# Kernel tuning notes

Hardware: AMD Instinct MI355X
Metric: run time of the kernel (lower is better)

The kernel has to match this reference:

```python
import jax, jax.numpy as jnp
import numpy as np


def setup_inputs() -> dict:
    key = jax.random.key(0)
    k1, k2 = jax.random.split(key)
    B, N, C = 128, 200000, 100
    values = jax.random.normal(k1, (B, N), dtype=jnp.float32)
    labels = jax.random.randint(k2, (N,), 0, C, dtype=jnp.int64)
    return {"values": values, "labels": labels, "num_classes": C}


def reference(values, labels, num_classes):
    # Stratified (label-grouped) max pooling:
    # values: [B, N], labels: [N] in [0, num_classes)
    # output: [B, num_classes], out[b, c] = max over columns j with labels[j] == c
    # segment_max reduces over the leading axis, so operate on values.T [N, B].
    pooled = jax.ops.segment_max(
        values.T, labels, num_segments=num_classes, indices_are_sorted=False
    )  # [C, B]
    return pooled.T  # [B, C]
```

## Files before the change

### kernel.cpp

```cpp
#include <hip/hip_runtime.h>
#include <hip/hip_bf16.h>


#define TPB   256
#define ROWS  8
#define CHUNK 4096
#define CPAD  257

#define ENC_NEG_INF 0x007FFFFFu

__device__ __forceinline__ unsigned enc(float f) {
    unsigned u = __float_as_uint(f);
    return (u & 0x80000000u) ? ~u : (u | 0x80000000u);
}
__device__ __forceinline__ float dec(unsigned u) {
    unsigned b = (u & 0x80000000u) ? (u & 0x7FFFFFFFu) : ~u;
    return __uint_as_float(b);
}

__global__ __launch_bounds__(TPB) void strat_init(unsigned* __restrict__ out_enc, int n) {
    int i = blockIdx.x * TPB + threadIdx.x;
    if (i < n) out_enc[i] = ENC_NEG_INF;
}

__global__ __launch_bounds__(TPB) void strat_main(
    const float* __restrict__ values, const int* __restrict__ labels,
    unsigned* __restrict__ out_enc, int B, int N, int C) {
    __shared__ unsigned acc[ROWS * CPAD];

    const int tid    = threadIdx.x;
    const int chunk0 = blockIdx.x * CHUNK;
    const int row0   = blockIdx.y * ROWS;

    for (int i = tid; i < ROWS * CPAD; i += TPB) acc[i] = ENC_NEG_INF;
    __syncthreads();

    const int rmax = min(ROWS, B - row0);
    const bool full_chunk = (chunk0 + CHUNK <= N);

    if (full_chunk) {
        int4 L[4];
#pragma unroll
        for (int k = 0; k < 4; ++k)
            L[k] = ((const int4*)(labels + chunk0 + k * 1024))[tid];

        if (rmax == ROWS) {
#pragma unroll
            for (int r = 0; r < ROWS; ++r) {
                const float4* src =
                    (const float4*)(values + (size_t)(row0 + r) * N + chunk0) + tid;
                float4 v[4];
#pragma unroll
                for (int k = 0; k < 4; ++k) v[k] = src[k * 256];
                unsigned* accr = acc + r * CPAD;
#pragma unroll
                for (int k = 0; k < 4; ++k) {
                    atomicMax(&accr[L[k].x], enc(v[k].x));
                    atomicMax(&accr[L[k].y], enc(v[k].y));
                    atomicMax(&accr[L[k].z], enc(v[k].z));
                    atomicMax(&accr[L[k].w], enc(v[k].w));
                }
            }
        } else {
            for (int r = 0; r < rmax; ++r) {
                const float4* src =
                    (const float4*)(values + (size_t)(row0 + r) * N + chunk0) + tid;
                float4 v[4];
#pragma unroll
                for (int k = 0; k < 4; ++k) v[k] = src[k * 256];
                unsigned* accr = acc + r * CPAD;
#pragma unroll
                for (int k = 0; k < 4; ++k) {
                    atomicMax(&accr[L[k].x], enc(v[k].x));
                    atomicMax(&accr[L[k].y], enc(v[k].y));
                    atomicMax(&accr[L[k].z], enc(v[k].z));
                    atomicMax(&accr[L[k].w], enc(v[k].w));
                }
            }
        }
    } else {
        for (int r = 0; r < rmax; ++r) {
            unsigned* accr = acc + r * CPAD;
            const size_t rowoff = (size_t)(row0 + r) * N;
            for (int k = 0; k < 4; ++k) {
                int j = chunk0 + k * 1024 + tid * 4;
#pragma unroll
                for (int e = 0; e < 4; ++e) {
                    if (j + e < N) {
                        int c = labels[j + e];
                        atomicMax(&accr[c], enc(values[rowoff + j + e]));
                    }
                }
            }
        }
    }

    __syncthreads();

    for (int i = tid; i < rmax * C; i += TPB) {
        int r = i / C, c = i - r * C;
        atomicMax(&out_enc[(size_t)(row0 + r) * C + c], acc[r * CPAD + c]);
    }
}

__global__ __launch_bounds__(TPB) void strat_decode(unsigned* __restrict__ buf, int n) {
    int i = blockIdx.x * TPB + threadIdx.x;
    if (i < n) {
        float f = dec(buf[i]);
        ((float*)buf)[i] = f;
    }
}

extern "C" void kernel_launch(void* const* d_in, const int* in_sizes, int n_in,
                              void* d_out, int out_size, void* d_ws, size_t ws_size,
                              hipStream_t stream) {
    const float* values = (const float*)d_in[0];
    const int*   labels = (const int*)d_in[1];
    const int N = in_sizes[1];
    const int B = in_sizes[0] / N;
    const int C = out_size / B;

    unsigned* out_enc = (unsigned*)d_out;

    int init_blocks = (out_size + TPB - 1) / TPB;
    strat_init<<<init_blocks, TPB, 0, stream>>>(out_enc, out_size);

    dim3 grid((N + CHUNK - 1) / CHUNK, (B + ROWS - 1) / ROWS);
    strat_main<<<grid, TPB, 0, stream>>>(values, labels, out_enc, B, N, C);

    strat_decode<<<init_blocks, TPB, 0, stream>>>(out_enc, out_size);
}
```

Baseline: 176.0 us.

## Use persistent split blocks with per-split partials and a separate reduce kernel

Swaps the fixed-chunk grid with global atomics for a grid of S=98 column splits by 16 row groups. Each block walks 1024-column tiles in a strided loop and keeps shared-memory max accumulators across tiles. Each split writes its partial maxima to workspace, and a second kernel reduces the partials and decodes the result, which removes the init kernel and the global atomics. The design issues all 8 row loads per tile up front to raise memory-level parallelism. The cost is a smaller grid of about 1568 blocks, an extra workspace pass, and an atomic fallback path that runs when the workspace is too small or C exceeds 128.

```diff
diff --git a/kernel.cpp b/kernel.cpp
--- a/kernel.cpp
+++ b/kernel.cpp
@@ -4,8 +4,7 @@
 
 #define TPB   256
 #define ROWS  8
-#define CHUNK 4096
-#define CPAD  257
+#define CACC  128
 
 #define ENC_NEG_INF 0x007FFFFFu
 
@@ -18,78 +17,56 @@
     return __uint_as_float(b);
 }
 
-__global__ __launch_bounds__(TPB) void strat_init(unsigned* __restrict__ out_enc, int n) {
-    int i = blockIdx.x * TPB + threadIdx.x;
-    if (i < n) out_enc[i] = ENC_NEG_INF;
-}
 
-__global__ __launch_bounds__(TPB) void strat_main(
+__global__ __launch_bounds__(TPB) void strat_part(
     const float* __restrict__ values, const int* __restrict__ labels,
-    unsigned* __restrict__ out_enc, int B, int N, int C) {
-    __shared__ unsigned acc[ROWS * CPAD];
+    unsigned* __restrict__ part, int B, int N, int C, int S, int T) {
+    __shared__ unsigned acc[ROWS * CACC];
 
-    const int tid    = threadIdx.x;
-    const int chunk0 = blockIdx.x * CHUNK;
-    const int row0   = blockIdx.y * ROWS;
+    const int tid  = threadIdx.x;
+    const int bx   = blockIdx.x;
+    const int row0 = blockIdx.y * ROWS;
+    const int rmax = min(ROWS, B - row0);
 
-    for (int i = tid; i < ROWS * CPAD; i += TPB) acc[i] = ENC_NEG_INF;
+    for (int i = tid; i < ROWS * CACC; i += TPB) acc[i] = ENC_NEG_INF;
     __syncthreads();
 
-    const int rmax = min(ROWS, B - row0);
-    const bool full_chunk = (chunk0 + CHUNK <= N);
-
-    if (full_chunk) {
-        int4 L[4];
+    for (int t = bx; t < T; t += S) {
+        const int base = t * 1024 + tid * 4;
+        if (t * 1024 + 1024 <= N) {
+            const int4 L = *(const int4*)(labels + base);
+            if (rmax == ROWS) {
+                float4 v[ROWS];
 #pragma unroll
-        for (int k = 0; k < 4; ++k)
-            L[k] = ((const int4*)(labels + chunk0 + k * 1024))[tid];
-
-        if (rmax == ROWS) {
+                for (int r = 0; r < ROWS; ++r)
+                    v[r] = *(const float4*)(values + (size_t)(row0 + r) * N + base);
 #pragma unroll
-            for (int r = 0; r < ROWS; ++r) {
-                const float4* src =
-                    (const float4*)(values + (size_t)(row0 + r) * N + chunk0) + tid;
-                float4 v[4];
-#pragma unroll
-                for (int k = 0; k < 4; ++k) v[k] = src[k * 256];
-                unsigned* accr = acc + r * CPAD;
-#pragma unroll
-                for (int k = 0; k < 4; ++k) {
-                    atomicMax(&accr[L[k].x], enc(v[k].x));
-                    atomicMax(&accr[L[k].y], enc(v[k].y));
-                    atomicMax(&accr[L[k].z], enc(v[k].z));
-                    atomicMax(&accr[L[k].w], enc(v[k].w));
+                for (int r = 0; r < ROWS; ++r) {
+                    unsigned* a = acc + r * CACC;
+                    atomicMax(&a[L.x], enc(v[r].x));
+                    atomicMax(&a[L.y], enc(v[r].y));
+                    atomicMax(&a[L.z], enc(v[r].z));
+                    atomicMax(&a[L.w], enc(v[r].w));
+                }
+            } else {
+                for (int r = 0; r < rmax; ++r) {
+                    float4 v = *(const float4*)(values + (size_t)(row0 + r) * N + base);
+                    unsigned* a = acc + r * CACC;
+                    atomicMax(&a[L.x], enc(v.x));
+                    atomicMax(&a[L.y], enc(v.y));
+                    atomicMax(&a[L.z], enc(v.z));
+                    atomicMax(&a[L.w], enc(v.w));
                 }
             }
         } else {
-            for (int r = 0; r < rmax; ++r) {
-                const float4* src =
-                    (const float4*)(values + (size_t)(row0 + r) * N + chunk0) + tid;
-                float4 v[4];
 #pragma unroll
-                for (int k = 0; k < 4; ++k) v[k] = src[k * 256];
-                unsigned* accr = acc + r * CPAD;
-#pragma unroll
-                for (int k = 0; k < 4; ++k) {
-                    atomicMax(&accr[L[k].x], enc(v[k].x));
-                    atomicMax(&accr[L[k].y], enc(v[k].y));
-                    atomicMax(&accr[L[k].z], enc(v[k].z));
-                    atomicMax(&accr[L[k].w], enc(v[k].w));
-                }
-            }
-        }
-    } else {
-        for (int r = 0; r < rmax; ++r) {
-            unsigned* accr = acc + r * CPAD;
-            const size_t rowoff = (size_t)(row0 + r) * N;
-            for (int k = 0; k < 4; ++k) {
-                int j = chunk0 + k * 1024 + tid * 4;
-#pragma unroll
-                for (int e = 0; e < 4; ++e) {
-                    if (j + e < N) {
-                        int c = labels[j + e];
-                        atomicMax(&accr[c], enc(values[rowoff + j + e]));
-                    }
+            for (int e = 0; e < 4; ++e) {
+                const int j = base + e;
+                if (j < N) {
+                    const int c = labels[j];
+                    for (int r = 0; r < rmax; ++r)
+                        atomicMax(&acc[r * CACC + c],
+                                  enc(values[(size_t)(row0 + r) * N + j]));
                 }
             }
         }
@@ -97,9 +74,56 @@
 
     __syncthreads();
 
+    unsigned* dst = part + (size_t)bx * B * C;
     for (int i = tid; i < rmax * C; i += TPB) {
-        int r = i / C, c = i - r * C;
-        atomicMax(&out_enc[(size_t)(row0 + r) * C + c], acc[r * CPAD + c]);
+        const int r = i / C, c = i - r * C;
+        dst[(size_t)(row0 + r) * C + c] = acc[r * CACC + c];
+    }
+}
+
+__global__ __launch_bounds__(TPB) void strat_reduce(
+    const unsigned* __restrict__ part, float* __restrict__ out, int BC, int S) {
+    const int i = blockIdx.x * TPB + threadIdx.x;
+    if (i >= BC) return;
+    unsigned m = ENC_NEG_INF;
+    for (int s = 0; s < S; ++s) m = max(m, part[(size_t)s * BC + i]);
+    out[i] = dec(m);
+}
+
+
+#define FCPAD 257
+
+__global__ __launch_bounds__(TPB) void strat_init(unsigned* __restrict__ out_enc, int n) {
+    int i = blockIdx.x * TPB + threadIdx.x;
+    if (i < n) out_enc[i] = ENC_NEG_INF;
+}
+
+__global__ __launch_bounds__(TPB) void strat_main_atomic(
+    const float* __restrict__ values, const int* __restrict__ labels,
+    unsigned* __restrict__ out_enc, int B, int N, int C, int T) {
+    __shared__ unsigned acc[ROWS * FCPAD];
+    const int tid  = threadIdx.x;
+    const int row0 = blockIdx.y * ROWS;
+    const int rmax = min(ROWS, B - row0);
+
+    for (int i = tid; i < ROWS * FCPAD; i += TPB) acc[i] = ENC_NEG_INF;
+    __syncthreads();
+
+    const int t = blockIdx.x;
+#pragma unroll
+    for (int e = 0; e < 4; ++e) {
+        const int j = t * 1024 + tid * 4 + e;
+        if (j < N) {
+            const int c = labels[j];
+            for (int r = 0; r < rmax; ++r)
+                atomicMax(&acc[r * FCPAD + c],
+                          enc(values[(size_t)(row0 + r) * N + j]));
+        }
+    }
+    __syncthreads();
+    for (int i = tid; i < rmax * C; i += TPB) {
+        const int r = i / C, c = i - r * C;
+        atomicMax(&out_enc[(size_t)(row0 + r) * C + c], acc[r * FCPAD + c]);
     }
 }
 
@@ -111,22 +135,39 @@
     }
 }
 
+
 extern "C" void kernel_launch(void* const* d_in, const int* in_sizes, int n_in,
                               void* d_out, int out_size, void* d_ws, size_t ws_size,
                               hipStream_t stream) {
     const float* values = (const float*)d_in[0];
     const int*   labels = (const int*)d_in[1];
-    const int N = in_sizes[1];
-    const int B = in_sizes[0] / N;
-    const int C = out_size / B;
+    const int N  = in_sizes[1];
+    const int B  = in_sizes[0] / N;
+    const int C  = out_size / B;
+    const int BC = B * C;
+    const int T  = (N + 1023) / 1024;
+    const int RG = (B + ROWS - 1) / ROWS;
 
-    unsigned* out_enc = (unsigned*)d_out;
+    int S = 98;
+    const size_t per_split = (size_t)BC * sizeof(unsigned);
+    if (per_split > 0 && (size_t)S * per_split > ws_size)
+        S = (int)(ws_size / per_split);
+    if (S > T) S = T;
 
-    int init_blocks = (out_size + TPB - 1) / TPB;
-    strat_init<<<init_blocks, TPB, 0, stream>>>(out_enc, out_size);
+    const bool main_ok = (S >= 1) && (C <= CACC) && (N % 4 == 0);
 
-    dim3 grid((N + CHUNK - 1) / CHUNK, (B + ROWS - 1) / ROWS);
-    strat_main<<<grid, TPB, 0, stream>>>(values, labels, out_enc, B, N, C);
-
-    strat_decode<<<init_blocks, TPB, 0, stream>>>(out_enc, out_size);
+    if (main_ok) {
+        unsigned* part = (unsigned*)d_ws;
+        dim3 grid(S, RG);
+        strat_part<<<grid, TPB, 0, stream>>>(values, labels, part, B, N, C, S, T);
+        strat_reduce<<<(BC + TPB - 1) / TPB, TPB, 0, stream>>>(
+            part, (float*)d_out, BC, S);
+    } else {
+        unsigned* out_enc = (unsigned*)d_out;
+        const int init_blocks = (out_size + TPB - 1) / TPB;
+        strat_init<<<init_blocks, TPB, 0, stream>>>(out_enc, out_size);
+        dim3 grid(T, RG);
+        strat_main_atomic<<<grid, TPB, 0, stream>>>(values, labels, out_enc, B, N, C, T);
+        strat_decode<<<init_blocks, TPB, 0, stream>>>(out_enc, out_size);
+    }
 }
```

Result: no change. 176.6 us (+0.4%).
